# Performance work log

Measured on AMD Instinct MI355X. Metric: run time of the kernel, lower is better.

The kernel has to match this reference:

```python
import jax, jax.numpy as jnp
import numpy as np

B, H, S = 128, 512, 2048

def setup_inputs() -> dict:
    key = jax.random.key(0)
    ks = jax.random.split(key, 8)
    sc = 1.0 / np.sqrt(H)
    return {
        "all_hidden": jax.random.normal(ks[0], (B, H, S), dtype=jnp.float32),
        "v_att": jax.random.normal(ks[1], (H,), dtype=jnp.float32) * sc,
        "W_att": jax.random.normal(ks[2], (H, H), dtype=jnp.float32) * sc,
        "v_ptr": jax.random.normal(ks[3], (H,), dtype=jnp.float32) * sc,
        "fc1_w": jax.random.normal(ks[4], (H, H), dtype=jnp.float32) * sc,
        "fc1_b": jax.random.normal(ks[5], (H,), dtype=jnp.float32) * sc,
        "fc2_w": jax.random.normal(ks[6], (H, H), dtype=jnp.float32) * sc,
        "fc2_b": jax.random.normal(ks[7], (H,), dtype=jnp.float32) * sc,
    }

def reference(all_hidden, v_att, W_att, v_ptr, fc1_w, fc1_b, fc2_w, fc2_b):
    # all_hidden: [B, H, S]
    # Attention: attns = softmax(v . tanh(W @ all_hidden), over seq)
    scores = jnp.einsum('hk,bks->bhs', W_att, all_hidden)          # [B,H,S]
    attn = jax.nn.softmax(jnp.einsum('h,bhs->bs', v_att, jnp.tanh(scores)), axis=-1)  # [B,S]
    # context = attn @ all_hidden^T  -> [B,H]
    context = jnp.einsum('bs,bhs->bh', attn, all_hidden)
    # 2-layer MLP with relu (torch Linear: x @ W^T + b)
    out = jax.nn.relu(context @ fc1_w.T + fc1_b)
    out = jax.nn.relu(out @ fc2_w.T + fc2_b)                        # [B,H]
    # probs = v . tanh(all_hidden + out broadcast over seq)
    probs = jnp.einsum('h,bhs->bs', v_ptr, jnp.tanh(all_hidden + out[:, :, None]))  # [B,S]
    return probs
```

## Files before the change

kernel.cpp:

```cpp
#include <hip/hip_runtime.h>
#include <hip/hip_bf16.h>

#define B_ 128
#define H_ 512
#define S_ 2048
#define ST 64
#define NP (S_/ST)

typedef short  bf16x8  __attribute__((ext_vector_type(8)));
typedef float  floatx4 __attribute__((ext_vector_type(4)));
typedef short  short4v __attribute__((ext_vector_type(4)));

__device__ __forceinline__ unsigned short f2bf(float f){
  unsigned u = __float_as_uint(f);
  unsigned r = (u + 0x7fffu + ((u >> 16) & 1u)) >> 16;
  return (unsigned short)r;
}
__device__ __forceinline__ float bf2f(unsigned short h){
  return __uint_as_float(((unsigned)h) << 16);
}
__device__ __forceinline__ float fast_tanh(float x){
  x = fminf(15.f, fmaxf(-15.f, x));
  float e = __expf(2.f * x);
  return (e - 1.f) * __builtin_amdgcn_rcpf(e + 1.f);
}
__device__ __forceinline__ int swz(int s, int c){
  return (c & 56) | ((c ^ s) & 7);
}

__global__ __launch_bounds__(256) void k_convW(const float* __restrict__ W,
                                               unsigned short* __restrict__ Wb){
  int i = (blockIdx.x * 256 + threadIdx.x) * 4;
  float4 v = *(const float4*)(W + i);
  short4v o;
  o[0] = (short)f2bf(v.x); o[1] = (short)f2bf(v.y);
  o[2] = (short)f2bf(v.z); o[3] = (short)f2bf(v.w);
  *(short4v*)(Wb + i) = o;
}

template<int WRITE_HT>
__global__ __launch_bounds__(512, 4) void k_pass1(
    const float* __restrict__ hidden, const float* __restrict__ v_att,
    const unsigned short* __restrict__ Wb,
    float* __restrict__ part_m, float* __restrict__ part_z,
    float* __restrict__ part_ctx, unsigned short* __restrict__ hT)
{
  __shared__ unsigned short Bs[ST * 512];
  __shared__ float vatt[H_];
  __shared__ float twav[8][ST];
  __shared__ float ts[ST];
  __shared__ float es[ST];

  const int tid = threadIdx.x;
  const int w = tid >> 6, l = tid & 63;
  const int p = blockIdx.x & (NP - 1);
  const int b = blockIdx.x >> 5;
  const int s0 = p * ST;

  vatt[tid] = v_att[tid];

  {
    const float* src0 = hidden + ((size_t)b * H_) * S_ + s0 + l;
    #pragma unroll
    for (int it = 0; it < 8; ++it){
      const int c = w + it * 8;
      const float* src = src0 + (size_t)(c * 8) * S_;
      bf16x8 pk;
      #pragma unroll
      for (int j = 0; j < 8; ++j)
        pk[j] = (short)f2bf(__builtin_nontemporal_load(src + (size_t)j * S_));
      *(bf16x8*)(&Bs[l * 512 + swz(l, c) * 8]) = pk;
    }
  }
  __syncthreads();

  if (WRITE_HT){
    #pragma unroll
    for (int r = 0; r < 8; ++r){
      const int s = w * 8 + r;
      bf16x8 v = *(const bf16x8*)(&Bs[s * 512 + swz(s, l) * 8]);
      __builtin_nontemporal_store(v,
          (bf16x8*)(hT + ((size_t)(b * S_) + s0 + s) * H_ + l * 8));
    }
  }

  const int quad = l >> 4, l16 = l & 15;
  float tacc[4] = {0.f, 0.f, 0.f, 0.f};

  {
    floatx4 acc[4][4];
    #pragma unroll
    for (int ti = 0; ti < 4; ++ti)
      #pragma unroll
      for (int ss = 0; ss < 4; ++ss){
        floatx4 z4 = {0.f, 0.f, 0.f, 0.f};
        acc[ti][ss] = z4;
      }

    for (int k0 = 0; k0 < H_; k0 += 32){
      bf16x8 a[4];
      #pragma unroll
      for (int ti = 0; ti < 4; ++ti)
        a[ti] = *(const bf16x8*)(Wb + ((w * 4 + ti) * 16 + l16) * H_ + k0 + quad * 8);
      bf16x8 bb[4];
      #pragma unroll
      for (int ss = 0; ss < 4; ++ss){
        const int c = (k0 >> 3) + quad;
        bb[ss] = *(const bf16x8*)(&Bs[(ss * 16 + l16) * 512 + swz(l16, c) * 8]);
      }
      #pragma unroll
      for (int ti = 0; ti < 4; ++ti)
        #pragma unroll
        for (int ss = 0; ss < 4; ++ss)
          acc[ti][ss] = __builtin_amdgcn_mfma_f32_16x16x32_bf16(a[ti], bb[ss], acc[ti][ss], 0, 0, 0);
    }

    #pragma unroll
    for (int ti = 0; ti < 4; ++ti){
      const int hbase = (w * 4 + ti) * 16 + quad * 4;
      #pragma unroll
      for (int r = 0; r < 4; ++r){
        float va = vatt[hbase + r];
        #pragma unroll
        for (int ss = 0; ss < 4; ++ss)
          tacc[ss] += va * fast_tanh(acc[ti][ss][r]);
      }
    }
  }

  #pragma unroll
  for (int ss = 0; ss < 4; ++ss){
    tacc[ss] += __shfl_xor(tacc[ss], 16);
    tacc[ss] += __shfl_xor(tacc[ss], 32);
  }
  if (l < 16){
    #pragma unroll
    for (int ss = 0; ss < 4; ++ss) twav[w][ss * 16 + l] = tacc[ss];
  }
  __syncthreads();
  if (tid < ST){
    float a = 0.f;
    #pragma unroll
    for (int ww = 0; ww < 8; ++ww) a += twav[ww][tid];
    ts[tid] = a;
  }
  __syncthreads();

  float m = -1e30f;
  for (int s = 0; s < ST; ++s) m = fmaxf(m, ts[s]);
  if (tid < ST) es[tid] = __expf(ts[tid] - m);
  __syncthreads();
  float z = 0.f;
  for (int s = 0; s < ST; ++s) z += es[s];

  const int pidx = b * NP + p;
  if (tid == 0){ part_m[pidx] = m; part_z[pidx] = z; }

  {
    const int c = tid >> 3, e = tid & 7;
    float a = 0.f;
    for (int s = 0; s < ST; ++s)
      a += es[s] * bf2f(Bs[s * 512 + swz(s, c) * 8 + e]);
    part_ctx[(size_t)pidx * H_ + tid] = a;
  }
}

__global__ __launch_bounds__(256) void k_mlp(
    const float* __restrict__ part_m, const float* __restrict__ part_z,
    const float* __restrict__ part_ctx,
    const float* __restrict__ fc1_w, const float* __restrict__ fc1_b,
    const float* __restrict__ fc2_w, const float* __restrict__ fc2_b,
    float* __restrict__ out2)
{
  __shared__ float ctx[H_];
  __shared__ float h1[H_];
  __shared__ float wp[NP];
  const int b = blockIdx.x, tid = threadIdx.x;

  float m = -1e30f;
  for (int pp = 0; pp < NP; ++pp) m = fmaxf(m, part_m[b * NP + pp]);
  if (tid < NP) wp[tid] = __expf(part_m[b * NP + tid] - m);
  __syncthreads();
  float z = 0.f;
  for (int pp = 0; pp < NP; ++pp) z += wp[pp] * part_z[b * NP + pp];
  float invz = 1.f / z;

  for (int h = tid; h < H_; h += 256){
    float a = 0.f;
    for (int pp = 0; pp < NP; ++pp) a += wp[pp] * part_ctx[(size_t)(b * NP + pp) * H_ + h];
    ctx[h] = a * invz;
  }
  __syncthreads();

  for (int i = tid; i < H_; i += 256){
    const float4* row = (const float4*)(fc1_w + (size_t)i * H_);
    float4 s4 = {0.f, 0.f, 0.f, 0.f};
    for (int j = 0; j < H_ / 4; ++j){
      float4 wv = row[j];
      s4.x += wv.x * ctx[4 * j];     s4.y += wv.y * ctx[4 * j + 1];
      s4.z += wv.z * ctx[4 * j + 2]; s4.w += wv.w * ctx[4 * j + 3];
    }
    h1[i] = fmaxf(fc1_b[i] + s4.x + s4.y + s4.z + s4.w, 0.f);
  }
  __syncthreads();

  for (int i = tid; i < H_; i += 256){
    const float4* row = (const float4*)(fc2_w + (size_t)i * H_);
    float4 s4 = {0.f, 0.f, 0.f, 0.f};
    for (int j = 0; j < H_ / 4; ++j){
      float4 wv = row[j];
      s4.x += wv.x * h1[4 * j];     s4.y += wv.y * h1[4 * j + 1];
      s4.z += wv.z * h1[4 * j + 2]; s4.w += wv.w * h1[4 * j + 3];
    }
    out2[(size_t)b * H_ + i] = fmaxf(fc2_b[i] + s4.x + s4.y + s4.z + s4.w, 0.f);
  }
}

__global__ __launch_bounds__(256) void k_probs_hT(
    const unsigned short* __restrict__ hT, const float* __restrict__ v_ptr,
    const float* __restrict__ out2, float* __restrict__ probs)
{
  const int tid = threadIdx.x, w = tid >> 6, l = tid & 63;
  const int b = blockIdx.y, s0 = blockIdx.x * 64;

  float vp[8], ob[8];
  {
    float4 a = *(const float4*)(v_ptr + l * 8);
    float4 c = *(const float4*)(v_ptr + l * 8 + 4);
    vp[0]=a.x; vp[1]=a.y; vp[2]=a.z; vp[3]=a.w;
    vp[4]=c.x; vp[5]=c.y; vp[6]=c.z; vp[7]=c.w;
    float4 d = *(const float4*)(out2 + (size_t)b * H_ + l * 8);
    float4 e = *(const float4*)(out2 + (size_t)b * H_ + l * 8 + 4);
    ob[0]=d.x; ob[1]=d.y; ob[2]=d.z; ob[3]=d.w;
    ob[4]=e.x; ob[5]=e.y; ob[6]=e.z; ob[7]=e.w;
  }

  const unsigned short* base = hT + (size_t)(b * S_ + s0) * H_ + l * 8;
  #pragma unroll 2
  for (int i = 0; i < 16; ++i){
    const int s = w * 16 + i;
    bf16x8 hv = __builtin_nontemporal_load((const bf16x8*)(base + (size_t)s * H_));
    float acc = 0.f;
    #pragma unroll
    for (int j = 0; j < 8; ++j)
      acc += vp[j] * fast_tanh(bf2f((unsigned short)hv[j]) + ob[j]);
    acc += __shfl_xor(acc, 1);  acc += __shfl_xor(acc, 2);
    acc += __shfl_xor(acc, 4);  acc += __shfl_xor(acc, 8);
    acc += __shfl_xor(acc, 16); acc += __shfl_xor(acc, 32);
    if (l == 0) probs[(size_t)b * S_ + s0 + s] = acc;
  }
}

__global__ __launch_bounds__(256) void k_probs_f32(
    const float* __restrict__ hidden, const float* __restrict__ v_ptr,
    const float* __restrict__ out2, float* __restrict__ probs)
{
  __shared__ float vp[H_], ob[H_];
  const int b = blockIdx.y, c = blockIdx.x, tid = threadIdx.x;
  vp[tid]       = v_ptr[tid];
  vp[tid + 256] = v_ptr[tid + 256];
  ob[tid]       = out2[(size_t)b * H_ + tid];
  ob[tid + 256] = out2[(size_t)b * H_ + tid + 256];
  __syncthreads();

  const int s = c * 512 + tid * 2;
  const float* base = hidden + (size_t)b * H_ * S_ + s;
  float a0 = 0.f, a1 = 0.f;
  #pragma unroll 4
  for (int h = 0; h < H_; ++h){
    float2 hv = *(const float2*)(base + (size_t)h * S_);
    float wv = vp[h], o = ob[h];
    a0 += wv * fast_tanh(hv.x + o);
    a1 += wv * fast_tanh(hv.y + o);
  }
  probs[(size_t)b * S_ + s]     = a0;
  probs[(size_t)b * S_ + s + 1] = a1;
}

extern "C" void kernel_launch(void* const* d_in, const int* in_sizes, int n_in,
                              void* d_out, int out_size, void* d_ws, size_t ws_size,
                              hipStream_t stream)
{
  const float* hidden = (const float*)d_in[0];
  const float* v_att  = (const float*)d_in[1];
  const float* W_att  = (const float*)d_in[2];
  const float* v_ptr  = (const float*)d_in[3];
  const float* fc1_w  = (const float*)d_in[4];
  const float* fc1_b  = (const float*)d_in[5];
  const float* fc2_w  = (const float*)d_in[6];
  const float* fc2_b  = (const float*)d_in[7];
  float* probs = (float*)d_out;

  char* ws = (char*)d_ws;
  unsigned short* Wb = (unsigned short*)ws;
  float* part_m   = (float*)(ws + (512u<<10));
  float* part_z   = (float*)(ws + (512u<<10) + (16u<<10));
  float* part_ctx = (float*)(ws + (512u<<10) + (32u<<10));
  float* out2     = (float*)(ws + (512u<<10) + (32u<<10) + (8u<<20));
  unsigned short* hT = (unsigned short*)(ws + (16u<<20));

  const size_t need = (16u<<20) + ((size_t)B_ * S_ * H_ * 2);

  hipLaunchKernelGGL(k_convW, dim3(256), dim3(256), 0, stream, W_att, Wb);

  if (ws_size >= need){
    hipLaunchKernelGGL(k_pass1<1>, dim3(B_ * NP), dim3(512), 0, stream,
                       hidden, v_att, Wb, part_m, part_z, part_ctx, hT);
    hipLaunchKernelGGL(k_mlp, dim3(B_), dim3(256), 0, stream,
                       part_m, part_z, part_ctx, fc1_w, fc1_b, fc2_w, fc2_b, out2);
    hipLaunchKernelGGL(k_probs_hT, dim3(S_/64, B_), dim3(256), 0, stream,
                       hT, v_ptr, out2, probs);
  } else {
    hipLaunchKernelGGL(k_pass1<0>, dim3(B_ * NP), dim3(512), 0, stream,
                       hidden, v_att, Wb, part_m, part_z, part_ctx, (unsigned short*)Wb);
    hipLaunchKernelGGL(k_mlp, dim3(B_), dim3(256), 0, stream,
                       part_m, part_z, part_ctx, fc1_w, fc1_b, fc2_w, fc2_b, out2);
    hipLaunchKernelGGL(k_probs_f32, dim3(4, B_), dim3(256), 0, stream,
                       hidden, v_ptr, out2, probs);
  }
}
```

Measured before the change: 1.040 ms.

## Drop bf16 transposed copy, read fp32 hidden in probs, simplify tanh algebra

Removes the bf16 transposed copy of hidden written in pass1 and always computes probs directly from the fp32 input. This cuts a 128 MB write plus read, at the cost of re-reading 512 MB of fp32 hidden with strided loads. The tanh is rewritten as sum(v) - 2*sum(v/(1+exp2(k x))), removing the clamp and a multiply per element. The context reduction in pass1 is also restructured into per-wave partial sums reduced through shared memory.

```diff
diff --git a/kernel.cpp b/kernel.cpp
--- a/kernel.cpp
+++ b/kernel.cpp
@@ -11,6 +11,8 @@
 typedef float  floatx4 __attribute__((ext_vector_type(4)));
 typedef short  short4v __attribute__((ext_vector_type(4)));
 
+#define KT_TANH 2.8853900817779268f
+
 __device__ __forceinline__ unsigned short f2bf(float f){
   unsigned u = __float_as_uint(f);
   unsigned r = (u + 0x7fffu + ((u >> 16) & 1u)) >> 16;
@@ -19,10 +21,9 @@
 __device__ __forceinline__ float bf2f(unsigned short h){
   return __uint_as_float(((unsigned)h) << 16);
 }
-__device__ __forceinline__ float fast_tanh(float x){
-  x = fminf(15.f, fmaxf(-15.f, x));
-  float e = __expf(2.f * x);
-  return (e - 1.f) * __builtin_amdgcn_rcpf(e + 1.f);
+__device__ __forceinline__ float tanh_r(float a){
+  float e = __builtin_amdgcn_exp2f(a);
+  return __builtin_amdgcn_rcpf(e + 1.f);
 }
 __device__ __forceinline__ int swz(int s, int c){
   return (c & 56) | ((c ^ s) & 7);
@@ -38,18 +39,22 @@
   *(short4v*)(Wb + i) = o;
 }
 
-template<int WRITE_HT>
 __global__ __launch_bounds__(512, 4) void k_pass1(
     const float* __restrict__ hidden, const float* __restrict__ v_att,
     const unsigned short* __restrict__ Wb,
     float* __restrict__ part_m, float* __restrict__ part_z,
-    float* __restrict__ part_ctx, unsigned short* __restrict__ hT)
+    float* __restrict__ part_ctx)
 {
-  __shared__ unsigned short Bs[ST * 512];
+  union __align__(16) SMem {
+    unsigned short Bs[ST * 512];
+    float pctx[8 * H_];
+  };
+  __shared__ SMem sm;
   __shared__ float vatt[H_];
   __shared__ float twav[8][ST];
   __shared__ float ts[ST];
   __shared__ float es[ST];
+  __shared__ float sva_sh;
 
   const int tid = threadIdx.x;
   const int w = tid >> 6, l = tid & 63;
@@ -69,19 +74,19 @@
       #pragma unroll
       for (int j = 0; j < 8; ++j)
         pk[j] = (short)f2bf(__builtin_nontemporal_load(src + (size_t)j * S_));
-      *(bf16x8*)(&Bs[l * 512 + swz(l, c) * 8]) = pk;
-    }
-  }
-  __syncthreads();
-
-  if (WRITE_HT){
-    #pragma unroll
-    for (int r = 0; r < 8; ++r){
-      const int s = w * 8 + r;
-      bf16x8 v = *(const bf16x8*)(&Bs[s * 512 + swz(s, l) * 8]);
-      __builtin_nontemporal_store(v,
-          (bf16x8*)(hT + ((size_t)(b * S_) + s0 + s) * H_ + l * 8));
-    }
+      *(bf16x8*)(&sm.Bs[l * 512 + swz(l, c) * 8]) = pk;
+    }
+  }
+  __syncthreads();
+
+  if (w == 0){
+    float sv = 0.f;
+    #pragma unroll
+    for (int k = 0; k < 8; ++k) sv += vatt[l + 64 * k];
+    sv += __shfl_xor(sv, 1);  sv += __shfl_xor(sv, 2);
+    sv += __shfl_xor(sv, 4);  sv += __shfl_xor(sv, 8);
+    sv += __shfl_xor(sv, 16); sv += __shfl_xor(sv, 32);
+    if (l == 0) sva_sh = sv;
   }
 
   const int quad = l >> 4, l16 = l & 15;
@@ -106,7 +111,7 @@
       #pragma unroll
       for (int ss = 0; ss < 4; ++ss){
         const int c = (k0 >> 3) + quad;
-        bb[ss] = *(const bf16x8*)(&Bs[(ss * 16 + l16) * 512 + swz(l16, c) * 8]);
+        bb[ss] = *(const bf16x8*)(&sm.Bs[(ss * 16 + l16) * 512 + swz(l16, c) * 8]);
       }
       #pragma unroll
       for (int ti = 0; ti < 4; ++ti)
@@ -123,7 +128,7 @@
         float va = vatt[hbase + r];
         #pragma unroll
         for (int ss = 0; ss < 4; ++ss)
-          tacc[ss] += va * fast_tanh(acc[ti][ss][r]);
+          tacc[ss] = fmaf(va, tanh_r(acc[ti][ss][r] * KT_TANH), tacc[ss]);
       }
     }
   }
@@ -142,7 +147,7 @@
     float a = 0.f;
     #pragma unroll
     for (int ww = 0; ww < 8; ++ww) a += twav[ww][tid];
-    ts[tid] = a;
+    ts[tid] = sva_sh - 2.f * a;
   }
   __syncthreads();
 
@@ -156,11 +161,28 @@
   const int pidx = b * NP + p;
   if (tid == 0){ part_m[pidx] = m; part_z[pidx] = z; }
 
+  float a8[8] = {0.f,0.f,0.f,0.f,0.f,0.f,0.f,0.f};
+  #pragma unroll
+  for (int j = 0; j < 8; ++j){
+    const int s = w * 8 + j;
+    const float ez = es[s];
+    bf16x8 v = *(const bf16x8*)(&sm.Bs[s * 512 + swz(s, l) * 8]);
+    #pragma unroll
+    for (int e = 0; e < 8; ++e)
+      a8[e] = fmaf(ez, bf2f((unsigned short)v[e]), a8[e]);
+  }
+  __syncthreads();
   {
-    const int c = tid >> 3, e = tid & 7;
+    floatx4 lo = {a8[0], a8[1], a8[2], a8[3]};
+    floatx4 hi = {a8[4], a8[5], a8[6], a8[7]};
+    *(floatx4*)(&sm.pctx[w * H_ + l * 8])     = lo;
+    *(floatx4*)(&sm.pctx[w * H_ + l * 8 + 4]) = hi;
+  }
+  __syncthreads();
+  {
     float a = 0.f;
-    for (int s = 0; s < ST; ++s)
-      a += es[s] * bf2f(Bs[s * 512 + swz(s, c) * 8 + e]);
+    #pragma unroll
+    for (int ww = 0; ww < 8; ++ww) a += sm.pctx[ww * H_ + tid];
     part_ctx[(size_t)pidx * H_ + tid] = a;
   }
 }
@@ -216,65 +238,43 @@
   }
 }
 
-__global__ __launch_bounds__(256) void k_probs_hT(
-    const unsigned short* __restrict__ hT, const float* __restrict__ v_ptr,
-    const float* __restrict__ out2, float* __restrict__ probs)
-{
-  const int tid = threadIdx.x, w = tid >> 6, l = tid & 63;
-  const int b = blockIdx.y, s0 = blockIdx.x * 64;
-
-  float vp[8], ob[8];
-  {
-    float4 a = *(const float4*)(v_ptr + l * 8);
-    float4 c = *(const float4*)(v_ptr + l * 8 + 4);
-    vp[0]=a.x; vp[1]=a.y; vp[2]=a.z; vp[3]=a.w;
-    vp[4]=c.x; vp[5]=c.y; vp[6]=c.z; vp[7]=c.w;
-    float4 d = *(const float4*)(out2 + (size_t)b * H_ + l * 8);
-    float4 e = *(const float4*)(out2 + (size_t)b * H_ + l * 8 + 4);
-    ob[0]=d.x; ob[1]=d.y; ob[2]=d.z; ob[3]=d.w;
-    ob[4]=e.x; ob[5]=e.y; ob[6]=e.z; ob[7]=e.w;
-  }
-
-  const unsigned short* base = hT + (size_t)(b * S_ + s0) * H_ + l * 8;
-  #pragma unroll 2
-  for (int i = 0; i < 16; ++i){
-    const int s = w * 16 + i;
-    bf16x8 hv = __builtin_nontemporal_load((const bf16x8*)(base + (size_t)s * H_));
-    float acc = 0.f;
-    #pragma unroll
-    for (int j = 0; j < 8; ++j)
-      acc += vp[j] * fast_tanh(bf2f((unsigned short)hv[j]) + ob[j]);
-    acc += __shfl_xor(acc, 1);  acc += __shfl_xor(acc, 2);
-    acc += __shfl_xor(acc, 4);  acc += __shfl_xor(acc, 8);
-    acc += __shfl_xor(acc, 16); acc += __shfl_xor(acc, 32);
-    if (l == 0) probs[(size_t)b * S_ + s0 + s] = acc;
-  }
-}
-
-__global__ __launch_bounds__(256) void k_probs_f32(
+__global__ __launch_bounds__(256) void k_probs(
     const float* __restrict__ hidden, const float* __restrict__ v_ptr,
     const float* __restrict__ out2, float* __restrict__ probs)
 {
-  __shared__ float vp[H_], ob[H_];
+  __shared__ float vp[H_], ko[H_];
+  __shared__ float svp_sh;
   const int b = blockIdx.y, c = blockIdx.x, tid = threadIdx.x;
   vp[tid]       = v_ptr[tid];
   vp[tid + 256] = v_ptr[tid + 256];
-  ob[tid]       = out2[(size_t)b * H_ + tid];
-  ob[tid + 256] = out2[(size_t)b * H_ + tid + 256];
+  ko[tid]       = KT_TANH * out2[(size_t)b * H_ + tid];
+  ko[tid + 256] = KT_TANH * out2[(size_t)b * H_ + tid + 256];
+  __syncthreads();
+  if (tid < 64){
+    float sv = 0.f;
+    #pragma unroll
+    for (int k = 0; k < 8; ++k) sv += vp[tid + 64 * k];
+    sv += __shfl_xor(sv, 1);  sv += __shfl_xor(sv, 2);
+    sv += __shfl_xor(sv, 4);  sv += __shfl_xor(sv, 8);
+    sv += __shfl_xor(sv, 16); sv += __shfl_xor(sv, 32);
+    if (tid == 0) svp_sh = sv;
+  }
   __syncthreads();
 
   const int s = c * 512 + tid * 2;
   const float* base = hidden + (size_t)b * H_ * S_ + s;
   float a0 = 0.f, a1 = 0.f;
-  #pragma unroll 4
+  const float kt = KT_TANH;
+  #pragma unroll 8
   for (int h = 0; h < H_; ++h){
     float2 hv = *(const float2*)(base + (size_t)h * S_);
-    float wv = vp[h], o = ob[h];
-    a0 += wv * fast_tanh(hv.x + o);
-    a1 += wv * fast_tanh(hv.y + o);
-  }
-  probs[(size_t)b * S_ + s]     = a0;
-  probs[(size_t)b * S_ + s + 1] = a1;
+    float wv = vp[h], o = ko[h];
+    a0 = fmaf(wv, tanh_r(fmaf(kt, hv.x, o)), a0);
+    a1 = fmaf(wv, tanh_r(fmaf(kt, hv.y, o)), a1);
+  }
+  float svp = svp_sh;
+  float2 r2 = { svp - 2.f * a0, svp - 2.f * a1 };
+  *(float2*)(probs + (size_t)b * S_ + s) = r2;
 }
 
 extern "C" void kernel_launch(void* const* d_in, const int* in_sizes, int n_in,
@@ -297,25 +297,12 @@
   float* part_z   = (float*)(ws + (512u<<10) + (16u<<10));
   float* part_ctx = (float*)(ws + (512u<<10) + (32u<<10));
   float* out2     = (float*)(ws + (512u<<10) + (32u<<10) + (8u<<20));
-  unsigned short* hT = (unsigned short*)(ws + (16u<<20));
-
-  const size_t need = (16u<<20) + ((size_t)B_ * S_ * H_ * 2);
 
   hipLaunchKernelGGL(k_convW, dim3(256), dim3(256), 0, stream, W_att, Wb);
-
-  if (ws_size >= need){
-    hipLaunchKernelGGL(k_pass1<1>, dim3(B_ * NP), dim3(512), 0, stream,
-                       hidden, v_att, Wb, part_m, part_z, part_ctx, hT);
-    hipLaunchKernelGGL(k_mlp, dim3(B_), dim3(256), 0, stream,
-                       part_m, part_z, part_ctx, fc1_w, fc1_b, fc2_w, fc2_b, out2);
-    hipLaunchKernelGGL(k_probs_hT, dim3(S_/64, B_), dim3(256), 0, stream,
-                       hT, v_ptr, out2, probs);
-  } else {
-    hipLaunchKernelGGL(k_pass1<0>, dim3(B_ * NP), dim3(512), 0, stream,
-                       hidden, v_att, Wb, part_m, part_z, part_ctx, (unsigned short*)Wb);
-    hipLaunchKernelGGL(k_mlp, dim3(B_), dim3(256), 0, stream,
-                       part_m, part_z, part_ctx, fc1_w, fc1_b, fc2_w, fc2_b, out2);
-    hipLaunchKernelGGL(k_probs_f32, dim3(4, B_), dim3(256), 0, stream,
-                       hidden, v_ptr, out2, probs);
-  }
-}
+  hipLaunchKernelGGL(k_pass1, dim3(B_ * NP), dim3(512), 0, stream,
+                     hidden, v_att, Wb, part_m, part_z, part_ctx);
+  hipLaunchKernelGGL(k_mlp, dim3(B_), dim3(256), 0, stream,
+                     part_m, part_z, part_ctx, fc1_w, fc1_b, fc2_w, fc2_b, out2);
+  hipLaunchKernelGGL(k_probs, dim3(S_ / 512, B_), dim3(256), 0, stream,
+                     hidden, v_ptr, out2, probs);
+}
```

New measurement: 1.060 ms. No clear change (+1.9%).
